# Optimization experiments

Hardware: AMD Instinct MI355X
Metric: run time of the kernel (lower is better)

Reference implementation:

```python
import jax, jax.numpy as jnp
import numpy as np

EMBED_DIM = 768
NUM_HEADS = 12
HEAD_DIM = EMBED_DIM // NUM_HEADS
SCALE = HEAD_DIM ** -0.5


def setup_inputs() -> dict:
    key = jax.random.key(0)
    k_x, k_wqkv, k_bqkv, k_wp, k_bp = jax.random.split(key, 5)
    B, N, D = 16, 1024, EMBED_DIM
    x = jax.random.normal(k_x, (B, N, D), dtype=jnp.float32)
    # nn.Linear default init: U(-1/sqrt(fan_in), 1/sqrt(fan_in))
    bound = 1.0 / np.sqrt(D)
    W_qkv = jax.random.uniform(k_wqkv, (D, 3 * D), minval=-bound, maxval=bound, dtype=jnp.float32)
    b_qkv = jax.random.uniform(k_bqkv, (3 * D,), minval=-bound, maxval=bound, dtype=jnp.float32)
    W_proj = jax.random.uniform(k_wp, (D, D), minval=-bound, maxval=bound, dtype=jnp.float32)
    b_proj = jax.random.uniform(k_bp, (D,), minval=-bound, maxval=bound, dtype=jnp.float32)
    return {"x": x, "W_qkv": W_qkv, "b_qkv": b_qkv, "W_proj": W_proj, "b_proj": b_proj}


def reference(x, W_qkv, b_qkv, W_proj, b_proj):
    B, N, D = x.shape
    H, Hd = NUM_HEADS, HEAD_DIM
    qkv = x @ W_qkv + b_qkv                      # [B, N, 3D]
    qkv = qkv.reshape(B, N, 3, H, Hd)
    qkv = jnp.transpose(qkv, (2, 0, 3, 1, 4))    # [3, B, H, N, Hd]
    q, k, v = qkv[0], qkv[1], qkv[2]
    attn = jnp.einsum('bhnd,bhmd->bhnm', q, k) * SCALE  # [B, H, N, N]
    attn = jax.nn.softmax(attn, axis=-1)
    out = jnp.einsum('bhnm,bhmd->bhnd', attn, v)        # [B, H, N, Hd]
    out = jnp.transpose(out, (0, 2, 1, 3)).reshape(B, N, D)
    return out @ W_proj + b_proj
```

## Files before the change

### kernel.cpp

```cpp
#include <hip/hip_runtime.h>
#include <math.h>

typedef _Float16 f16;
typedef _Float16 f16x8 __attribute__((ext_vector_type(8)));
typedef _Float16 f16x4 __attribute__((ext_vector_type(4)));
typedef float    f32x4 __attribute__((ext_vector_type(4)));

#define AS1 __attribute__((address_space(1)))
#define AS3 __attribute__((address_space(3)))

#define QSCALE 0.1803368800f

__device__ __forceinline__ void gload16(const void* g, void* l) {
    __builtin_amdgcn_global_load_lds((const AS1 void*)g, (AS3 void*)l, 16, 0, 0);
}

__global__ __launch_bounds__(256) void cast_x_k(const float* __restrict__ in,
                                                f16* __restrict__ out, int n8)
{
    int i = blockIdx.x * 256 + threadIdx.x;
    const int stride = gridDim.x * 256;
    const float4* in4 = (const float4*)in;
    f16x8* o8 = (f16x8*)out;
    for (; i < n8; i += stride) {
        float4 a = in4[2 * i], b = in4[2 * i + 1];
        f16x8 o = {(f16)a.x, (f16)a.y, (f16)a.z, (f16)a.w,
                   (f16)b.x, (f16)b.y, (f16)b.z, (f16)b.w};
        o8[i] = o;
    }
}

__global__ __launch_bounds__(256) void castT_k(const float* __restrict__ W,
                                               f16* __restrict__ WT, int K, int N)
{
    __shared__ float tile[32][33];
    const int k0 = blockIdx.y * 32, n0 = blockIdx.x * 32;
    const int t = threadIdx.x;
    const int r = t >> 3, cq = t & 7;
    float4 v = *(const float4*)&W[(size_t)(k0 + r) * N + n0 + cq * 4];
    tile[r][cq * 4 + 0] = v.x; tile[r][cq * 4 + 1] = v.y;
    tile[r][cq * 4 + 2] = v.z; tile[r][cq * 4 + 3] = v.w;
    __syncthreads();
    f16x4 pk = {(f16)tile[cq * 4 + 0][r], (f16)tile[cq * 4 + 1][r],
                (f16)tile[cq * 4 + 2][r], (f16)tile[cq * 4 + 3][r]};
    *(f16x4*)&WT[(size_t)(n0 + r) * K + k0 + cq * 4] = pk;
}

#define GEMM_MAIN(APTR, BTPTR)                                                   \
    __shared__ __align__(16) f16 As[2][128 * 64];                                \
    __shared__ __align__(16) f16 Bs[2][128 * 64];                                \
    const int t = threadIdx.x, lid = t & 63, wid = t >> 6;                       \
    const int wr = wid >> 1, wc = wid & 1;                                       \
    const int g = lid >> 4, cl = lid & 15;                                       \
    const int bm = blockIdx.y, bn = blockIdx.x;                                  \
    f32x4 acc[4][4] = {};                                                        \
    const int srow8 = lid >> 3;                                                  \
    const int sc = (lid & 7) ^ srow8;                                            \
    const f16* aG = (APTR) + (size_t)(bm * 128 + wid * 32 + srow8) * 768 + sc * 8;\
    const f16* bG = (BTPTR) + (size_t)(bn * 128 + wid * 32 + srow8) * 768 + sc * 8;\
    const int ldsoff = wid * 32 * 64;                                            \
    _Pragma("unroll")                                                            \
    for (int c = 0; c < 4; ++c) {                                                \
        gload16(aG + c * 8 * 768, &As[0][ldsoff + c * 8 * 64]);                  \
        gload16(bG + c * 8 * 768, &Bs[0][ldsoff + c * 8 * 64]);                  \
    }                                                                            \
    for (int kt = 0; kt < 12; ++kt) {                                            \
        const int tn = kt + 1;                                                   \
        if (tn < 12) {                                                           \
            _Pragma("unroll")                                                    \
            for (int c = 0; c < 4; ++c) {                                        \
                gload16(aG + c * 8 * 768 + tn * 64, &As[tn & 1][ldsoff + c * 8 * 64]); \
                gload16(bG + c * 8 * 768 + tn * 64, &Bs[tn & 1][ldsoff + c * 8 * 64]); \
            }                                                                    \
            asm volatile("s_waitcnt vmcnt(8)" ::: "memory");                     \
        } else {                                                                 \
            asm volatile("s_waitcnt vmcnt(0)" ::: "memory");                     \
        }                                                                        \
        __builtin_amdgcn_s_barrier();                                            \
        asm volatile("" ::: "memory");                                           \
        const f16* As_ = &As[kt & 1][0];                                         \
        const f16* Bs_ = &Bs[kt & 1][0];                                         \
        _Pragma("unroll")                                                        \
        for (int kh = 0; kh < 2; ++kh) {                                         \
            f16x8 af[4], bf[4];                                                  \
            _Pragma("unroll")                                                    \
            for (int m = 0; m < 4; ++m) {                                        \
                int row = wr * 64 + m * 16 + cl;                                 \
                int slot = (kh * 4 + g) ^ (row & 7);                             \
                af[m] = *(const f16x8*)&As_[row * 64 + slot * 8];                \
                int col = wc * 64 + m * 16 + cl;                                 \
                int slotb = (kh * 4 + g) ^ (col & 7);                            \
                bf[m] = *(const f16x8*)&Bs_[col * 64 + slotb * 8];               \
            }                                                                    \
            __builtin_amdgcn_s_setprio(1);                                       \
            _Pragma("unroll")                                                    \
            for (int m = 0; m < 4; ++m)                                          \
                _Pragma("unroll")                                                \
                for (int n = 0; n < 4; ++n)                                      \
                    acc[m][n] = __builtin_amdgcn_mfma_f32_16x16x32_f16(          \
                        af[m], bf[n], acc[m][n], 0, 0, 0);                       \
            __builtin_amdgcn_s_setprio(0);                                       \
        }                                                                        \
        asm volatile("" ::: "memory");                                           \
        __builtin_amdgcn_s_barrier();                                            \
    }

__global__ __launch_bounds__(256)
void qkv_gemm16(const f16* __restrict__ A, const f16* __restrict__ BT,
                const float* __restrict__ bias,
                f16* __restrict__ qws, f16* __restrict__ kws, f16* __restrict__ vt)
{
    GEMM_MAIN(A, BT)
#pragma unroll
    for (int m = 0; m < 4; ++m) {
        int rbase = bm * 128 + wr * 64 + m * 16 + g * 4;
#pragma unroll
        for (int n = 0; n < 4; ++n) {
            int cg = bn * 128 + wc * 64 + n * 16 + cl;
            float bb = bias[cg];
            int which = cg / 768;
            int rem = cg - which * 768;
            int h = rem >> 6, d = rem & 63;
            if (which == 2) {
                int b = rbase >> 10, tok = rbase & 1023;
                f16x4 pk = {(f16)(acc[m][n][0] + bb), (f16)(acc[m][n][1] + bb),
                            (f16)(acc[m][n][2] + bb), (f16)(acc[m][n][3] + bb)};
                *(f16x4*)&vt[((size_t)(b * 12 + h) * 64 + d) * 1024 + tok] = pk;
            } else {
                f16* dst = which ? kws : qws;
                float scl = which ? 1.0f : QSCALE;
#pragma unroll
                for (int r = 0; r < 4; ++r) {
                    int row = rbase + r;
                    int b = row >> 10, tok = row & 1023;
                    dst[((size_t)(b * 12 + h) * 1024 + tok) * 64 + d] =
                        (f16)((acc[m][n][r] + bb) * scl);
                }
            }
        }
    }
}

__global__ __launch_bounds__(256)
void proj_gemm16(const f16* __restrict__ A, const f16* __restrict__ BT,
                 const float* __restrict__ bias, float* __restrict__ C)
{
    GEMM_MAIN(A, BT)
#pragma unroll
    for (int m = 0; m < 4; ++m) {
        int rbase = bm * 128 + wr * 64 + m * 16 + g * 4;
#pragma unroll
        for (int n = 0; n < 4; ++n) {
            int cg = bn * 128 + wc * 64 + n * 16 + cl;
            float bb = bias[cg];
#pragma unroll
            for (int r = 0; r < 4; ++r)
                C[(size_t)(rbase + r) * 768 + cg] = acc[m][n][r] + bb;
        }
    }
}

__global__ __launch_bounds__(256)
void attn16(const f16* __restrict__ Q, const f16* __restrict__ K,
            const f16* __restrict__ VT, f16* __restrict__ AO)
{
    __shared__ __align__(16) f16 kbuf[2][64 * 64];
    __shared__ __align__(16) f16 vbuf[2][64 * 64];
    __shared__ __align__(16) f16 plds[4][16 * 64];

    const int t = threadIdx.x, lid = t & 63, wid = t >> 6;
    const int phys = blockIdx.y * gridDim.x + blockIdx.x;
    const int logical = (phys & 7) * 384 + (phys >> 3);
    const int bh = logical >> 4, qt = logical & 15;

    const int g = lid >> 4, c = lid & 15;
    const size_t hb = (size_t)bh * (1024 * 64);
    const int q0 = qt * 64 + wid * 16;

    const f16* qrow = Q + hb + (size_t)(q0 + c) * 64;
    const f16x8 qf0 = *(const f16x8*)(qrow + g * 8);
    const f16x8 qf1 = *(const f16x8*)(qrow + 32 + g * 8);

    const int srow   = wid * 16 + (lid >> 3);
    const int schunk = ((lid & 7) ^ (lid >> 3)) * 8;

#define ATTN_STAGE(BUF, KT)                                                      \
    {                                                                            \
        const f16* kb_ = K + hb + (size_t)((KT) * 64) * 64;                      \
        const f16* vb_ = VT + hb + (KT) * 64;                                    \
        _Pragma("unroll")                                                        \
        for (int c2 = 0; c2 < 2; ++c2) {                                         \
            gload16(kb_ + (size_t)(srow + c2 * 8) * 64 + schunk,                 \
                    &kbuf[BUF][wid * 1024 + c2 * 512]);                          \
            gload16(vb_ + (size_t)(srow + c2 * 8) * 1024 + schunk,               \
                    &vbuf[BUF][wid * 1024 + c2 * 512]);                          \
        }                                                                        \
    }

    f32x4 o[4] = {};
    float mrun = -INFINITY, lrun = 0.f;
    f16* myp = &plds[wid][0];

    ATTN_STAGE(0, 0)
    __syncthreads();

    int cur = 0;
    for (int kt = 0; kt < 16; ++kt) {
        if (kt < 15) ATTN_STAGE(cur ^ 1, kt + 1)

        const f16* kcur = &kbuf[cur][0];
        const f16* vcur = &vbuf[cur][0];
        const int sw = c & 7;

        f32x4 s[4] = {};
        __builtin_amdgcn_s_setprio(1);
#pragma unroll
        for (int m = 0; m < 4; ++m) {
            const int row = m * 16 + c;
            f16x8 k0f = *(const f16x8*)&kcur[row * 64 + ((g) ^ sw) * 8];
            f16x8 k1f = *(const f16x8*)&kcur[row * 64 + ((4 + g) ^ sw) * 8];
            s[m] = __builtin_amdgcn_mfma_f32_16x16x32_f16(k0f, qf0, s[m], 0, 0, 0);
            s[m] = __builtin_amdgcn_mfma_f32_16x16x32_f16(k1f, qf1, s[m], 0, 0, 0);
        }
        __builtin_amdgcn_s_setprio(0);

        float a0 = fmaxf(fmaxf(s[0][0], s[0][1]), fmaxf(s[0][2], s[0][3]));
        float a1 = fmaxf(fmaxf(s[1][0], s[1][1]), fmaxf(s[1][2], s[1][3]));
        float a2 = fmaxf(fmaxf(s[2][0], s[2][1]), fmaxf(s[2][2], s[2][3]));
        float a3 = fmaxf(fmaxf(s[3][0], s[3][1]), fmaxf(s[3][2], s[3][3]));
        float tmax = fmaxf(fmaxf(a0, a1), fmaxf(a2, a3));
        tmax = fmaxf(tmax, __shfl_xor(tmax, 16));
        tmax = fmaxf(tmax, __shfl_xor(tmax, 32));

        bool keep = __all(tmax - mrun <= 8.0f);
        float mnew = fmaxf(mrun, tmax);
        float mref = keep ? mrun : mnew;

        float ps = 0.f;
        float pe[4][4];
#pragma unroll
        for (int m = 0; m < 4; ++m)
#pragma unroll
            for (int r = 0; r < 4; ++r) {
                float p = __builtin_exp2f(s[m][r] - mref);
                pe[m][r] = p; ps += p;
            }
        ps += __shfl_xor(ps, 16);
        ps += __shfl_xor(ps, 32);

        if (keep) {
            lrun += ps;
        } else {
            float al = __builtin_exp2f(mrun - mnew);
            float al4[4];
#pragma unroll
            for (int r = 0; r < 4; ++r) al4[r] = __shfl(al, g * 4 + r);
#pragma unroll
            for (int n = 0; n < 4; ++n) {
                o[n][0] *= al4[0]; o[n][1] *= al4[1];
                o[n][2] *= al4[2]; o[n][3] *= al4[3];
            }
            lrun = lrun * al + ps;
            mrun = mnew;
        }

#pragma unroll
        for (int m = 0; m < 4; ++m) {
            f16x4 pk = {(f16)pe[m][0], (f16)pe[m][1], (f16)pe[m][2], (f16)pe[m][3]};
            int slot = (2 * m + (g >> 1)) ^ sw;
            *(f16x4*)&myp[c * 64 + slot * 8 + (g & 1) * 4] = pk;
        }
        f16x8 pa[2];
#pragma unroll
        for (int kh = 0; kh < 2; ++kh) {
            int slot = (kh * 4 + g) ^ sw;
            pa[kh] = *(const f16x8*)&myp[c * 64 + slot * 8];
        }
        __builtin_amdgcn_s_setprio(1);
#pragma unroll
        for (int kh = 0; kh < 2; ++kh)
#pragma unroll
            for (int n = 0; n < 4; ++n) {
                const int row = n * 16 + c;
                f16x8 vf = *(const f16x8*)&vcur[row * 64 + ((kh * 4 + g) ^ sw) * 8];
                o[n] = __builtin_amdgcn_mfma_f32_16x16x32_f16(pa[kh], vf, o[n], 0, 0, 0);
            }
        __builtin_amdgcn_s_setprio(0);

        __syncthreads();
        cur ^= 1;
    }

    float il = 1.0f / lrun;
    float il4[4];
#pragma unroll
    for (int r = 0; r < 4; ++r) il4[r] = __shfl(il, g * 4 + r);
    const int b = bh / 12, h = bh - b * 12;
#pragma unroll
    for (int n = 0; n < 4; ++n)
#pragma unroll
        for (int r = 0; r < 4; ++r) {
            int tok = q0 + g * 4 + r;
            AO[(size_t)(b * 1024 + tok) * 768 + h * 64 + n * 16 + c] =
                (f16)(o[n][r] * il4[r]);
        }
}


extern "C" void kernel_launch(void* const* d_in, const int* in_sizes, int n_in,
                              void* d_out, int out_size, void* d_ws, size_t ws_size,
                              hipStream_t stream)
{
    const float* x      = (const float*)d_in[0];
    const float* W_qkv  = (const float*)d_in[1];
    const float* b_qkv  = (const float*)d_in[2];
    const float* W_proj = (const float*)d_in[3];
    const float* b_proj = (const float*)d_in[4];
    float* out = (float*)d_out;

    const size_t per = (size_t)16 * 1024 * 768;
    f16* x16    = (f16*)d_ws;
    f16* wqkvT  = x16 + per;
    f16* wprojT = wqkvT + (size_t)768 * 2304;
    f16* qws    = wprojT + (size_t)768 * 768;
    f16* kws    = qws + per;
    f16* vt     = kws + per;
    f16* aws    = vt + per;

    cast_x_k<<<3072, 256, 0, stream>>>(x, x16, (int)(per / 8));
    castT_k<<<dim3(2304 / 32, 768 / 32), 256, 0, stream>>>(W_qkv, wqkvT, 768, 2304);
    castT_k<<<dim3(768 / 32, 768 / 32), 256, 0, stream>>>(W_proj, wprojT, 768, 768);
    qkv_gemm16<<<dim3(18, 128), 256, 0, stream>>>(x16, wqkvT, b_qkv, qws, kws, vt);
    attn16<<<dim3(16, 192), 256, 0, stream>>>(qws, kws, vt, aws);
    proj_gemm16<<<dim3(6, 128), 256, 0, stream>>>(aws, wprojT, b_proj, out);
}
```

Before: 357.1 us.

## Double query rows per attention wave and simplify GEMM to single-buffered LDS

The attention kernel now has each wave process two 16-row query groups (128 queries per block, half the grid), so every K/V fragment read from LDS feeds twice as many MFMAs. The lazy-rescale softmax shortcut is dropped in favour of always rescaling, and the setprio hints are removed. Separately, the shared GEMM loop loses its double-buffered prefetch and becomes a load, sync, compute loop with half the LDS. The attention change targets LDS bandwidth and K/V reload cost, but the GEMM change exposes global-load latency that was previously overlapped with compute.

```diff
diff --git a/kernel.cpp b/kernel.cpp
--- a/kernel.cpp
+++ b/kernel.cpp
@@ -47,8 +47,8 @@
 }
 
 #define GEMM_MAIN(APTR, BTPTR)                                                   \
-    __shared__ __align__(16) f16 As[2][128 * 64];                                \
-    __shared__ __align__(16) f16 Bs[2][128 * 64];                                \
+    __shared__ __align__(16) f16 As[128 * 64];                                   \
+    __shared__ __align__(16) f16 Bs[128 * 64];                                   \
     const int t = threadIdx.x, lid = t & 63, wid = t >> 6;                       \
     const int wr = wid >> 1, wc = wid & 1;                                       \
     const int g = lid >> 4, cl = lid & 15;                                       \
@@ -58,28 +58,16 @@
     const int sc = (lid & 7) ^ srow8;                                            \
     const f16* aG = (APTR) + (size_t)(bm * 128 + wid * 32 + srow8) * 768 + sc * 8;\
     const f16* bG = (BTPTR) + (size_t)(bn * 128 + wid * 32 + srow8) * 768 + sc * 8;\
-    const int ldsoff = wid * 32 * 64;                                            \
-    _Pragma("unroll")                                                            \
-    for (int c = 0; c < 4; ++c) {                                                \
-        gload16(aG + c * 8 * 768, &As[0][ldsoff + c * 8 * 64]);                  \
-        gload16(bG + c * 8 * 768, &Bs[0][ldsoff + c * 8 * 64]);                  \
-    }                                                                            \
-    for (int kt = 0; kt < 12; ++kt) {                                            \
-        const int tn = kt + 1;                                                   \
-        if (tn < 12) {                                                           \
-            _Pragma("unroll")                                                    \
-            for (int c = 0; c < 4; ++c) {                                        \
-                gload16(aG + c * 8 * 768 + tn * 64, &As[tn & 1][ldsoff + c * 8 * 64]); \
-                gload16(bG + c * 8 * 768 + tn * 64, &Bs[tn & 1][ldsoff + c * 8 * 64]); \
-            }                                                                    \
-            asm volatile("s_waitcnt vmcnt(8)" ::: "memory");                     \
-        } else {                                                                 \
-            asm volatile("s_waitcnt vmcnt(0)" ::: "memory");                     \
-        }                                                                        \
-        __builtin_amdgcn_s_barrier();                                            \
-        asm volatile("" ::: "memory");                                           \
-        const f16* As_ = &As[kt & 1][0];                                         \
-        const f16* Bs_ = &Bs[kt & 1][0];                                         \
+    f16* ldsA = As + wid * 32 * 64;                                              \
+    f16* ldsB = Bs + wid * 32 * 64;                                              \
+    for (int k0 = 0; k0 < 768; k0 += 64) {                                       \
+        __syncthreads();                                                         \
+        _Pragma("unroll")                                                        \
+        for (int c = 0; c < 4; ++c) {                                            \
+            gload16(aG + c * 8 * 768 + k0, ldsA + c * 8 * 64);                   \
+            gload16(bG + c * 8 * 768 + k0, ldsB + c * 8 * 64);                   \
+        }                                                                        \
+        __syncthreads();                                                         \
         _Pragma("unroll")                                                        \
         for (int kh = 0; kh < 2; ++kh) {                                         \
             f16x8 af[4], bf[4];                                                  \
@@ -87,22 +75,18 @@
             for (int m = 0; m < 4; ++m) {                                        \
                 int row = wr * 64 + m * 16 + cl;                                 \
                 int slot = (kh * 4 + g) ^ (row & 7);                             \
-                af[m] = *(const f16x8*)&As_[row * 64 + slot * 8];                \
+                af[m] = *(const f16x8*)&As[row * 64 + slot * 8];                 \
                 int col = wc * 64 + m * 16 + cl;                                 \
                 int slotb = (kh * 4 + g) ^ (col & 7);                            \
-                bf[m] = *(const f16x8*)&Bs_[col * 64 + slotb * 8];               \
+                bf[m] = *(const f16x8*)&Bs[col * 64 + slotb * 8];                \
             }                                                                    \
-            __builtin_amdgcn_s_setprio(1);                                       \
             _Pragma("unroll")                                                    \
             for (int m = 0; m < 4; ++m)                                          \
                 _Pragma("unroll")                                                \
                 for (int n = 0; n < 4; ++n)                                      \
                     acc[m][n] = __builtin_amdgcn_mfma_f32_16x16x32_f16(          \
                         af[m], bf[n], acc[m][n], 0, 0, 0);                       \
-            __builtin_amdgcn_s_setprio(0);                                       \
-        }                                                                        \
-        asm volatile("" ::: "memory");                                           \
-        __builtin_amdgcn_s_barrier();                                            \
+        }                                                                        \
     }
 
 __global__ __launch_bounds__(256)
@@ -166,20 +150,23 @@
 {
     __shared__ __align__(16) f16 kbuf[2][64 * 64];
     __shared__ __align__(16) f16 vbuf[2][64 * 64];
-    __shared__ __align__(16) f16 plds[4][16 * 64];
+    __shared__ __align__(16) f16 plds[4][2][16 * 64];
 
     const int t = threadIdx.x, lid = t & 63, wid = t >> 6;
     const int phys = blockIdx.y * gridDim.x + blockIdx.x;
-    const int logical = (phys & 7) * 384 + (phys >> 3);
-    const int bh = logical >> 4, qt = logical & 15;
+    const int logical = (phys & 7) * 192 + (phys >> 3);
+    const int bh = logical >> 3, qt = logical & 7;
 
     const int g = lid >> 4, c = lid & 15;
     const size_t hb = (size_t)bh * (1024 * 64);
-    const int q0 = qt * 64 + wid * 16;
-
-    const f16* qrow = Q + hb + (size_t)(q0 + c) * 64;
-    const f16x8 qf0 = *(const f16x8*)(qrow + g * 8);
-    const f16x8 qf1 = *(const f16x8*)(qrow + 32 + g * 8);
+    const int q0 = qt * 128 + wid * 32;
+
+    const f16* qrowA = Q + hb + (size_t)(q0 + c) * 64;
+    const f16* qrowB = qrowA + 16 * 64;
+    const f16x8 qfA0 = *(const f16x8*)(qrowA + g * 8);
+    const f16x8 qfA1 = *(const f16x8*)(qrowA + 32 + g * 8);
+    const f16x8 qfB0 = *(const f16x8*)(qrowB + g * 8);
+    const f16x8 qfB1 = *(const f16x8*)(qrowB + 32 + g * 8);
 
     const int srow   = wid * 16 + (lid >> 3);
     const int schunk = ((lid & 7) ^ (lid >> 3)) * 8;
@@ -197,9 +184,51 @@
         }                                                                        \
     }
 
-    f32x4 o[4] = {};
-    float mrun = -INFINITY, lrun = 0.f;
-    f16* myp = &plds[wid][0];
+#define SOFTMAX_GRP(S, MRUN, LRUN, O, MYP)                                       \
+    {                                                                            \
+        float a0 = fmaxf(fmaxf(S[0][0], S[0][1]), fmaxf(S[0][2], S[0][3]));      \
+        float a1 = fmaxf(fmaxf(S[1][0], S[1][1]), fmaxf(S[1][2], S[1][3]));      \
+        float a2 = fmaxf(fmaxf(S[2][0], S[2][1]), fmaxf(S[2][2], S[2][3]));      \
+        float a3 = fmaxf(fmaxf(S[3][0], S[3][1]), fmaxf(S[3][2], S[3][3]));      \
+        float tmax = fmaxf(fmaxf(a0, a1), fmaxf(a2, a3));                        \
+        tmax = fmaxf(tmax, __shfl_xor(tmax, 16));                                \
+        tmax = fmaxf(tmax, __shfl_xor(tmax, 32));                                \
+        float mnew = fmaxf(MRUN, tmax);                                          \
+        float al = __builtin_exp2f(MRUN - mnew);                                 \
+        float ps = 0.f;                                                          \
+        float pe[4][4];                                                          \
+        _Pragma("unroll")                                                        \
+        for (int m = 0; m < 4; ++m)                                              \
+            _Pragma("unroll")                                                    \
+            for (int r = 0; r < 4; ++r) {                                        \
+                float p = __builtin_exp2f(S[m][r] - mnew);                       \
+                pe[m][r] = p; ps += p;                                           \
+            }                                                                    \
+        ps += __shfl_xor(ps, 16);                                                \
+        ps += __shfl_xor(ps, 32);                                                \
+        LRUN = LRUN * al + ps;                                                   \
+        MRUN = mnew;                                                             \
+        float al4[4];                                                            \
+        _Pragma("unroll")                                                        \
+        for (int r = 0; r < 4; ++r) al4[r] = __shfl(al, g * 4 + r);              \
+        _Pragma("unroll")                                                        \
+        for (int n = 0; n < 4; ++n) {                                            \
+            O[n][0] *= al4[0]; O[n][1] *= al4[1];                                \
+            O[n][2] *= al4[2]; O[n][3] *= al4[3];                                \
+        }                                                                        \
+        _Pragma("unroll")                                                        \
+        for (int m = 0; m < 4; ++m) {                                            \
+            f16x4 pk = {(f16)pe[m][0], (f16)pe[m][1],                            \
+                        (f16)pe[m][2], (f16)pe[m][3]};                           \
+            int slot = (2 * m + (g >> 1)) ^ sw;                                  \
+            *(f16x4*)&(MYP)[c * 64 + slot * 8 + (g & 1) * 4] = pk;               \
+        }                                                                        \
+    }
+
+    f32x4 oA[4] = {}, oB[4] = {};
+    float mA = -INFINITY, lA = 0.f, mB = -INFINITY, lB = 0.f;
+    f16* mypA = &plds[wid][0][0];
+    f16* mypB = &plds[wid][1][0];
 
     ATTN_STAGE(0, 0)
     __syncthreads();
@@ -212,98 +241,71 @@
         const f16* vcur = &vbuf[cur][0];
         const int sw = c & 7;
 
-        f32x4 s[4] = {};
-        __builtin_amdgcn_s_setprio(1);
+        f32x4 sA[4] = {}, sB[4] = {};
 #pragma unroll
         for (int m = 0; m < 4; ++m) {
             const int row = m * 16 + c;
             f16x8 k0f = *(const f16x8*)&kcur[row * 64 + ((g) ^ sw) * 8];
             f16x8 k1f = *(const f16x8*)&kcur[row * 64 + ((4 + g) ^ sw) * 8];
-            s[m] = __builtin_amdgcn_mfma_f32_16x16x32_f16(k0f, qf0, s[m], 0, 0, 0);
-            s[m] = __builtin_amdgcn_mfma_f32_16x16x32_f16(k1f, qf1, s[m], 0, 0, 0);
+            sA[m] = __builtin_amdgcn_mfma_f32_16x16x32_f16(k0f, qfA0, sA[m], 0, 0, 0);
+            sA[m] = __builtin_amdgcn_mfma_f32_16x16x32_f16(k1f, qfA1, sA[m], 0, 0, 0);
+            sB[m] = __builtin_amdgcn_mfma_f32_16x16x32_f16(k0f, qfB0, sB[m], 0, 0, 0);
+            sB[m] = __builtin_amdgcn_mfma_f32_16x16x32_f16(k1f, qfB1, sB[m], 0, 0, 0);
         }
-        __builtin_amdgcn_s_setprio(0);
-
-        float a0 = fmaxf(fmaxf(s[0][0], s[0][1]), fmaxf(s[0][2], s[0][3]));
-        float a1 = fmaxf(fmaxf(s[1][0], s[1][1]), fmaxf(s[1][2], s[1][3]));
-        float a2 = fmaxf(fmaxf(s[2][0], s[2][1]), fmaxf(s[2][2], s[2][3]));
-        float a3 = fmaxf(fmaxf(s[3][0], s[3][1]), fmaxf(s[3][2], s[3][3]));
-        float tmax = fmaxf(fmaxf(a0, a1), fmaxf(a2, a3));
-        tmax = fmaxf(tmax, __shfl_xor(tmax, 16));
-        tmax = fmaxf(tmax, __shfl_xor(tmax, 32));
-
-        bool keep = __all(tmax - mrun <= 8.0f);
-        float mnew = fmaxf(mrun, tmax);
-        float mref = keep ? mrun : mnew;
-
-        float ps = 0.f;
-        float pe[4][4];
-#pragma unroll
-        for (int m = 0; m < 4; ++m)
-#pragma unroll
-            for (int r = 0; r < 4; ++r) {
-                float p = __builtin_exp2f(s[m][r] - mref);
-                pe[m][r] = p; ps += p;
-            }
-        ps += __shfl_xor(ps, 16);
-        ps += __shfl_xor(ps, 32);
-
-        if (keep) {
-            lrun += ps;
-        } else {
-            float al = __builtin_exp2f(mrun - mnew);
-            float al4[4];
-#pragma unroll
-            for (int r = 0; r < 4; ++r) al4[r] = __shfl(al, g * 4 + r);
-#pragma unroll
-            for (int n = 0; n < 4; ++n) {
-                o[n][0] *= al4[0]; o[n][1] *= al4[1];
-                o[n][2] *= al4[2]; o[n][3] *= al4[3];
-            }
-            lrun = lrun * al + ps;
-            mrun = mnew;
-        }
-
-#pragma unroll
-        for (int m = 0; m < 4; ++m) {
-            f16x4 pk = {(f16)pe[m][0], (f16)pe[m][1], (f16)pe[m][2], (f16)pe[m][3]};
-            int slot = (2 * m + (g >> 1)) ^ sw;
-            *(f16x4*)&myp[c * 64 + slot * 8 + (g & 1) * 4] = pk;
-        }
-        f16x8 pa[2];
+
+        SOFTMAX_GRP(sA, mA, lA, oA, mypA)
+        SOFTMAX_GRP(sB, mB, lB, oB, mypB)
+
+        f16x8 paA[2], paB[2];
 #pragma unroll
         for (int kh = 0; kh < 2; ++kh) {
             int slot = (kh * 4 + g) ^ sw;
-            pa[kh] = *(const f16x8*)&myp[c * 64 + slot * 8];
+            paA[kh] = *(const f16x8*)&mypA[c * 64 + slot * 8];
+            paB[kh] = *(const f16x8*)&mypB[c * 64 + slot * 8];
         }
-        __builtin_amdgcn_s_setprio(1);
 #pragma unroll
         for (int kh = 0; kh < 2; ++kh)
 #pragma unroll
             for (int n = 0; n < 4; ++n) {
                 const int row = n * 16 + c;
                 f16x8 vf = *(const f16x8*)&vcur[row * 64 + ((kh * 4 + g) ^ sw) * 8];
-                o[n] = __builtin_amdgcn_mfma_f32_16x16x32_f16(pa[kh], vf, o[n], 0, 0, 0);
+                oA[n] = __builtin_amdgcn_mfma_f32_16x16x32_f16(paA[kh], vf, oA[n], 0, 0, 0);
+                oB[n] = __builtin_amdgcn_mfma_f32_16x16x32_f16(paB[kh], vf, oB[n], 0, 0, 0);
             }
-        __builtin_amdgcn_s_setprio(0);
 
         __syncthreads();
         cur ^= 1;
     }
 
-    float il = 1.0f / lrun;
-    float il4[4];
-#pragma unroll
-    for (int r = 0; r < 4; ++r) il4[r] = __shfl(il, g * 4 + r);
     const int b = bh / 12, h = bh - b * 12;
-#pragma unroll
-    for (int n = 0; n < 4; ++n)
-#pragma unroll
-        for (int r = 0; r < 4; ++r) {
-            int tok = q0 + g * 4 + r;
-            AO[(size_t)(b * 1024 + tok) * 768 + h * 64 + n * 16 + c] =
-                (f16)(o[n][r] * il4[r]);
-        }
+    {
+        float il = 1.0f / lA;
+        float il4[4];
+#pragma unroll
+        for (int r = 0; r < 4; ++r) il4[r] = __shfl(il, g * 4 + r);
+#pragma unroll
+        for (int n = 0; n < 4; ++n)
+#pragma unroll
+            for (int r = 0; r < 4; ++r) {
+                int tok = q0 + g * 4 + r;
+                AO[(size_t)(b * 1024 + tok) * 768 + h * 64 + n * 16 + c] =
+                    (f16)(oA[n][r] * il4[r]);
+            }
+    }
+    {
+        float il = 1.0f / lB;
+        float il4[4];
+#pragma unroll
+        for (int r = 0; r < 4; ++r) il4[r] = __shfl(il, g * 4 + r);
+#pragma unroll
+        for (int n = 0; n < 4; ++n)
+#pragma unroll
+            for (int r = 0; r < 4; ++r) {
+                int tok = q0 + 16 + g * 4 + r;
+                AO[(size_t)(b * 1024 + tok) * 768 + h * 64 + n * 16 + c] =
+                    (f16)(oB[n][r] * il4[r]);
+            }
+    }
 }
 
 
@@ -331,6 +333,6 @@
     castT_k<<<dim3(2304 / 32, 768 / 32), 256, 0, stream>>>(W_qkv, wqkvT, 768, 2304);
     castT_k<<<dim3(768 / 32, 768 / 32), 256, 0, stream>>>(W_proj, wprojT, 768, 768);
     qkv_gemm16<<<dim3(18, 128), 256, 0, stream>>>(x16, wqkvT, b_qkv, qws, kws, vt);
-    attn16<<<dim3(16, 192), 256, 0, stream>>>(qws, kws, vt, aws);
+    attn16<<<dim3(8, 192), 256, 0, stream>>>(qws, kws, vt, aws);
     proj_gemm16<<<dim3(6, 128), 256, 0, stream>>>(aws, wprojT, b_proj, out);
 }
```

Result: no change. 356.0 us (-0.3%).

## Drop GEMM double buffering, lazy softmax rescale and setprio; precompute attention offsets

Applied to the files above, without the earlier changes.

The GEMM main loop goes from a double-buffered LDS pipeline with async prefetch and a partial vmcnt wait to a single buffer, where every tile load is bracketed by two __syncthreads, so loads no longer overlap MFMA work. The attention kernel removes the lazy-rescale threshold and now rescales the output accumulators on every tile. It also removes the s_setprio hints and precomputes the swizzled LDS offsets into per-thread arrays. The changes read like a simplification or partial revert; they cut LDS use and scalar work but give up load/compute overlap and add per-tile rescale work.

```diff
diff --git a/kernel.cpp b/kernel.cpp
--- a/kernel.cpp
+++ b/kernel.cpp
@@ -47,8 +47,8 @@
 }
 
 #define GEMM_MAIN(APTR, BTPTR)                                                   \
-    __shared__ __align__(16) f16 As[2][128 * 64];                                \
-    __shared__ __align__(16) f16 Bs[2][128 * 64];                                \
+    __shared__ __align__(16) f16 As[128 * 64];                                   \
+    __shared__ __align__(16) f16 Bs[128 * 64];                                   \
     const int t = threadIdx.x, lid = t & 63, wid = t >> 6;                       \
     const int wr = wid >> 1, wc = wid & 1;                                       \
     const int g = lid >> 4, cl = lid & 15;                                       \
@@ -58,28 +58,16 @@
     const int sc = (lid & 7) ^ srow8;                                            \
     const f16* aG = (APTR) + (size_t)(bm * 128 + wid * 32 + srow8) * 768 + sc * 8;\
     const f16* bG = (BTPTR) + (size_t)(bn * 128 + wid * 32 + srow8) * 768 + sc * 8;\
-    const int ldsoff = wid * 32 * 64;                                            \
-    _Pragma("unroll")                                                            \
-    for (int c = 0; c < 4; ++c) {                                                \
-        gload16(aG + c * 8 * 768, &As[0][ldsoff + c * 8 * 64]);                  \
-        gload16(bG + c * 8 * 768, &Bs[0][ldsoff + c * 8 * 64]);                  \
-    }                                                                            \
-    for (int kt = 0; kt < 12; ++kt) {                                            \
-        const int tn = kt + 1;                                                   \
-        if (tn < 12) {                                                           \
-            _Pragma("unroll")                                                    \
-            for (int c = 0; c < 4; ++c) {                                        \
-                gload16(aG + c * 8 * 768 + tn * 64, &As[tn & 1][ldsoff + c * 8 * 64]); \
-                gload16(bG + c * 8 * 768 + tn * 64, &Bs[tn & 1][ldsoff + c * 8 * 64]); \
-            }                                                                    \
-            asm volatile("s_waitcnt vmcnt(8)" ::: "memory");                     \
-        } else {                                                                 \
-            asm volatile("s_waitcnt vmcnt(0)" ::: "memory");                     \
+    f16* ldsA = As + wid * 32 * 64;                                              \
+    f16* ldsB = Bs + wid * 32 * 64;                                              \
+    for (int k0 = 0; k0 < 768; k0 += 64) {                                       \
+        __syncthreads();                                                         \
+        _Pragma("unroll")                                                        \
+        for (int c = 0; c < 4; ++c) {                                            \
+            gload16(aG + c * 8 * 768 + k0, ldsA + c * 8 * 64);                   \
+            gload16(bG + c * 8 * 768 + k0, ldsB + c * 8 * 64);                   \
         }                                                                        \
-        __builtin_amdgcn_s_barrier();                                            \
-        asm volatile("" ::: "memory");                                           \
-        const f16* As_ = &As[kt & 1][0];                                         \
-        const f16* Bs_ = &Bs[kt & 1][0];                                         \
+        __syncthreads();                                                         \
         _Pragma("unroll")                                                        \
         for (int kh = 0; kh < 2; ++kh) {                                         \
             f16x8 af[4], bf[4];                                                  \
@@ -87,22 +75,18 @@
             for (int m = 0; m < 4; ++m) {                                        \
                 int row = wr * 64 + m * 16 + cl;                                 \
                 int slot = (kh * 4 + g) ^ (row & 7);                             \
-                af[m] = *(const f16x8*)&As_[row * 64 + slot * 8];                \
+                af[m] = *(const f16x8*)&As[row * 64 + slot * 8];                 \
                 int col = wc * 64 + m * 16 + cl;                                 \
                 int slotb = (kh * 4 + g) ^ (col & 7);                            \
-                bf[m] = *(const f16x8*)&Bs_[col * 64 + slotb * 8];               \
+                bf[m] = *(const f16x8*)&Bs[col * 64 + slotb * 8];                \
             }                                                                    \
-            __builtin_amdgcn_s_setprio(1);                                       \
             _Pragma("unroll")                                                    \
             for (int m = 0; m < 4; ++m)                                          \
                 _Pragma("unroll")                                                \
                 for (int n = 0; n < 4; ++n)                                      \
                     acc[m][n] = __builtin_amdgcn_mfma_f32_16x16x32_f16(          \
                         af[m], bf[n], acc[m][n], 0, 0, 0);                       \
-            __builtin_amdgcn_s_setprio(0);                                       \
         }                                                                        \
-        asm volatile("" ::: "memory");                                           \
-        __builtin_amdgcn_s_barrier();                                            \
     }
 
 __global__ __launch_bounds__(256)
@@ -197,6 +181,22 @@
         }                                                                        \
     }
 
+    const int sw = c & 7;
+    int koff[4][2], voff[2][4], poff[4], paoff[2];
+#pragma unroll
+    for (int m = 0; m < 4; ++m) {
+        koff[m][0] = (m * 16 + c) * 64 + ((g) ^ sw) * 8;
+        koff[m][1] = (m * 16 + c) * 64 + ((4 + g) ^ sw) * 8;
+        poff[m]    = c * 64 + ((2 * m + (g >> 1)) ^ sw) * 8 + (g & 1) * 4;
+    }
+#pragma unroll
+    for (int kh = 0; kh < 2; ++kh) {
+        paoff[kh] = c * 64 + ((kh * 4 + g) ^ sw) * 8;
+#pragma unroll
+        for (int n = 0; n < 4; ++n)
+            voff[kh][n] = (n * 16 + c) * 64 + ((kh * 4 + g) ^ sw) * 8;
+    }
+
     f32x4 o[4] = {};
     float mrun = -INFINITY, lrun = 0.f;
     f16* myp = &plds[wid][0];
@@ -210,19 +210,15 @@
 
         const f16* kcur = &kbuf[cur][0];
         const f16* vcur = &vbuf[cur][0];
-        const int sw = c & 7;
 
         f32x4 s[4] = {};
-        __builtin_amdgcn_s_setprio(1);
 #pragma unroll
         for (int m = 0; m < 4; ++m) {
-            const int row = m * 16 + c;
-            f16x8 k0f = *(const f16x8*)&kcur[row * 64 + ((g) ^ sw) * 8];
-            f16x8 k1f = *(const f16x8*)&kcur[row * 64 + ((4 + g) ^ sw) * 8];
+            f16x8 k0f = *(const f16x8*)&kcur[koff[m][0]];
+            f16x8 k1f = *(const f16x8*)&kcur[koff[m][1]];
             s[m] = __builtin_amdgcn_mfma_f32_16x16x32_f16(k0f, qf0, s[m], 0, 0, 0);
             s[m] = __builtin_amdgcn_mfma_f32_16x16x32_f16(k1f, qf1, s[m], 0, 0, 0);
         }
-        __builtin_amdgcn_s_setprio(0);
 
         float a0 = fmaxf(fmaxf(s[0][0], s[0][1]), fmaxf(s[0][2], s[0][3]));
         float a1 = fmaxf(fmaxf(s[1][0], s[1][1]), fmaxf(s[1][2], s[1][3]));
@@ -232,60 +228,48 @@
         tmax = fmaxf(tmax, __shfl_xor(tmax, 16));
         tmax = fmaxf(tmax, __shfl_xor(tmax, 32));
 
-        bool keep = __all(tmax - mrun <= 8.0f);
         float mnew = fmaxf(mrun, tmax);
-        float mref = keep ? mrun : mnew;
-
+        float al = __builtin_exp2f(mrun - mnew);
         float ps = 0.f;
         float pe[4][4];
 #pragma unroll
         for (int m = 0; m < 4; ++m)
 #pragma unroll
             for (int r = 0; r < 4; ++r) {
-                float p = __builtin_exp2f(s[m][r] - mref);
+                float p = __builtin_exp2f(s[m][r] - mnew);
                 pe[m][r] = p; ps += p;
             }
         ps += __shfl_xor(ps, 16);
         ps += __shfl_xor(ps, 32);
-
-        if (keep) {
-            lrun += ps;
-        } else {
-            float al = __builtin_exp2f(mrun - mnew);
-            float al4[4];
-#pragma unroll
-            for (int r = 0; r < 4; ++r) al4[r] = __shfl(al, g * 4 + r);
-#pragma unroll
-            for (int n = 0; n < 4; ++n) {
-                o[n][0] *= al4[0]; o[n][1] *= al4[1];
-                o[n][2] *= al4[2]; o[n][3] *= al4[3];
-            }
-            lrun = lrun * al + ps;
-            mrun = mnew;
+        lrun = lrun * al + ps;
+        mrun = mnew;
+
+        float al4[4];
+#pragma unroll
+        for (int r = 0; r < 4; ++r) al4[r] = __shfl(al, g * 4 + r);
+#pragma unroll
+        for (int n = 0; n < 4; ++n) {
+            o[n][0] *= al4[0]; o[n][1] *= al4[1];
+            o[n][2] *= al4[2]; o[n][3] *= al4[3];
         }
 
 #pragma unroll
         for (int m = 0; m < 4; ++m) {
             f16x4 pk = {(f16)pe[m][0], (f16)pe[m][1], (f16)pe[m][2], (f16)pe[m][3]};
-            int slot = (2 * m + (g >> 1)) ^ sw;
-            *(f16x4*)&myp[c * 64 + slot * 8 + (g & 1) * 4] = pk;
+            *(f16x4*)&myp[poff[m]] = pk;
         }
         f16x8 pa[2];
 #pragma unroll
-        for (int kh = 0; kh < 2; ++kh) {
-            int slot = (kh * 4 + g) ^ sw;
-            pa[kh] = *(const f16x8*)&myp[c * 64 + slot * 8];
-        }
-        __builtin_amdgcn_s_setprio(1);
-#pragma unroll
         for (int kh = 0; kh < 2; ++kh)
+            pa[kh] = *(const f16x8*)&myp[paoff[kh]];
+
+#pragma unroll
+        for (int kh = 0; kh < 2; ++kh)
 #pragma unroll
             for (int n = 0; n < 4; ++n) {
-                const int row = n * 16 + c;
-                f16x8 vf = *(const f16x8*)&vcur[row * 64 + ((kh * 4 + g) ^ sw) * 8];
+                f16x8 vf = *(const f16x8*)&vcur[voff[kh][n]];
                 o[n] = __builtin_amdgcn_mfma_f32_16x16x32_f16(pa[kh], vf, o[n], 0, 0, 0);
             }
-        __builtin_amdgcn_s_setprio(0);
 
         __syncthreads();
         cur ^= 1;
```

New measurement: 349.0 us. 1.02x faster.
